# Kernel tuning notes

Hardware: AMD Instinct MI355X
Metric: run time of the kernel (lower is better)

Reference implementation:

```python
import jax, jax.numpy as jnp
import numpy as np

D_LOW = 32
LAGS = [1, 2, 4, 8]
# Upper-triangular pair indices (offset=1), matching torch.triu_indices(d_low, d_low, 1)
IDX_I, IDX_J = np.triu_indices(D_LOW, k=1)
IDX_I = jnp.asarray(IDX_I)
IDX_J = jnp.asarray(IDX_J)
EPS = 1e-6


def setup_inputs() -> dict:
    key = jax.random.key(0)
    ks = jax.random.split(key, 7)
    b, n, d_model = 4, 4096, 1024
    d_plucker = D_LOW * (D_LOW - 1) // 2  # 496
    s = lambda fan_in: 1.0 / np.sqrt(fan_in)
    return {
        "x": jax.random.normal(ks[0], (b, n, d_model), dtype=jnp.float32),
        "W_red": jax.random.normal(ks[1], (d_model, D_LOW), dtype=jnp.float32) * s(d_model),
        "b_red": jax.random.normal(ks[2], (D_LOW,), dtype=jnp.float32) * s(d_model),
        "W_exp": jax.random.normal(ks[3], (d_plucker, d_model), dtype=jnp.float32) * s(d_plucker),
        "b_exp": jax.random.normal(ks[4], (d_model,), dtype=jnp.float32) * s(d_plucker),
        "W_gate": jax.random.normal(ks[5], (2 * d_model, d_model), dtype=jnp.float32) * s(2 * d_model),
        "b_gate": jax.random.normal(ks[6], (d_model,), dtype=jnp.float32) * s(2 * d_model),
    }


def reference(x, W_red, b_red, W_exp, b_exp, W_gate, b_gate):
    b, n, _ = x.shape
    d_plucker = D_LOW * (D_LOW - 1) // 2
    z = x @ W_red + b_red  # [b, n, d_low]
    plucker_total = jnp.zeros((b, n, d_plucker), dtype=x.dtype)
    counts = jnp.zeros((b, n, 1), dtype=x.dtype)
    for lag in LAGS:
        if lag <= 0 or lag >= n:
            continue
        z_curr = z[:, lag:, :]   # [b, n-lag, d_low]
        z_past = z[:, :-lag, :]  # [b, n-lag, d_low]
        # Antisymmetric Plucker coordinates over upper-triangular index pairs
        p = (z_curr[:, :, IDX_I] * z_past[:, :, IDX_J]
             - z_curr[:, :, IDX_J] * z_past[:, :, IDX_I])  # [b, n-lag, d_plucker]
        norm = jnp.linalg.norm(p, axis=-1, keepdims=True)
        p = p / jnp.maximum(norm, EPS)
        plucker_total = plucker_total.at[:, lag:, :].add(p)
        counts = counts.at[:, lag:, :].add(1.0)
    counts = jnp.maximum(counts, 1.0)
    plucker_avg = plucker_total / counts
    g_avg = plucker_avg @ W_exp + b_exp  # [b, n, d_model]
    concat = jnp.concatenate([x, g_avg], axis=-1)  # [b, n, 2*d_model]
    gate = jax.nn.sigmoid(concat @ W_gate + b_gate)
    return gate * x + (1.0 - gate) * g_avg
```

## Files before the change

kernel.cpp:

```cpp
#include <hip/hip_runtime.h>
#include <hip/hip_bf16.h>
#include <math.h>

#define B_DIM   4
#define N_DIM   4096
#define D_MODEL 1024
#define D_LOW   32
#define NPAIR   496
#define NROWS   (B_DIM * N_DIM)
#define KPAD3   512
#define LDA2    1536

typedef __bf16 bf16;
typedef __bf16 bf16x8 __attribute__((ext_vector_type(8)));
typedef __bf16 bf16x4 __attribute__((ext_vector_type(4)));
typedef float  f32x4  __attribute__((ext_vector_type(4)));

#define GLOAD_LDS16(g, l) __builtin_amdgcn_global_load_lds( \
    (__attribute__((address_space(1))) void*)(g),           \
    (__attribute__((address_space(3))) void*)(l), 16, 0, 0)

__global__ __launch_bounds__(256) void prep_misc(const float* __restrict__ Wr,
                                                 bf16* __restrict__ WrT,
                                                 const float* __restrict__ We,
                                                 const float* __restrict__ be,
                                                 bf16* __restrict__ WeB) {
    __shared__ float tile[32][33];
    const int bx = blockIdx.x;
    const int t  = threadIdx.x;
    if (bx < 32) {
        const int kb = bx * 32;
        {
            int k = t >> 3, c4 = (t & 7) * 4;
            float4 v = *reinterpret_cast<const float4*>(&Wr[(size_t)(kb + k) * 32 + c4]);
            tile[k][c4 + 0] = v.x; tile[k][c4 + 1] = v.y;
            tile[k][c4 + 2] = v.z; tile[k][c4 + 3] = v.w;
        }
        __syncthreads();
        {
            int c = t >> 3, kq = (t & 7) * 4;
            bf16x4 o = { (bf16)tile[kq + 0][c], (bf16)tile[kq + 1][c],
                         (bf16)tile[kq + 2][c], (bf16)tile[kq + 3][c] };
            *reinterpret_cast<bf16x4*>(&WrT[(size_t)c * 1024 + kb + kq]) = o;
        }
    } else {
        size_t o = ((size_t)(bx - 32) * 256 + t) * 4;
        int row = (int)(o >> 10), col = (int)(o & 1023);
        float4 v = {0.f, 0.f, 0.f, 0.f};
        if (row < NPAIR)       v = *reinterpret_cast<const float4*>(&We[(size_t)row * 1024 + col]);
        else if (row == NPAIR) v = *reinterpret_cast<const float4*>(&be[col]);
        bf16x4 b = { (bf16)v.x, (bf16)v.y, (bf16)v.z, (bf16)v.w };
        *reinterpret_cast<bf16x4*>(&WeB[o]) = b;
    }
}

__global__ __launch_bounds__(256) void k1_mfma(const float* __restrict__ x,
                                               const bf16* __restrict__ WrT,
                                               bf16* __restrict__ a2,
                                               float* __restrict__ zpart) {
    const int t    = threadIdx.x;
    const int wv   = t >> 6, lane = t & 63;
    const int l15  = lane & 15, lhi = lane >> 4;
    const int kc   = blockIdx.x;
    const int mt   = blockIdx.y;
    const int row  = mt * 64 + wv * 16 + l15;
    const int kb   = kc * 256;

    f32x4 accz[2] = { (f32x4){0.f,0.f,0.f,0.f}, (f32x4){0.f,0.f,0.f,0.f} };

#pragma unroll
    for (int ks = 0; ks < 8; ++ks) {
        const int k0 = kb + ks * 32 + lhi * 8;
        const float4 u0 = *reinterpret_cast<const float4*>(&x[(size_t)row * 1024 + k0]);
        const float4 u1 = *reinterpret_cast<const float4*>(&x[(size_t)row * 1024 + k0 + 4]);
        bf16x8 af = { (bf16)u0.x, (bf16)u0.y, (bf16)u0.z, (bf16)u0.w,
                      (bf16)u1.x, (bf16)u1.y, (bf16)u1.z, (bf16)u1.w };
        *reinterpret_cast<bf16x8*>(&a2[(size_t)row * LDA2 + k0]) = af;
        const bf16x8 b0 = *reinterpret_cast<const bf16x8*>(
            &WrT[(size_t)l15 * 1024 + kb + ks * 32 + lhi * 8]);
        const bf16x8 b1 = *reinterpret_cast<const bf16x8*>(
            &WrT[(size_t)(16 + l15) * 1024 + kb + ks * 32 + lhi * 8]);
        accz[0] = __builtin_amdgcn_mfma_f32_16x16x32_bf16(af, b0, accz[0], 0, 0, 0);
        accz[1] = __builtin_amdgcn_mfma_f32_16x16x32_bf16(af, b1, accz[1], 0, 0, 0);
    }
#pragma unroll
    for (int cg = 0; cg < 2; ++cg)
#pragma unroll
        for (int r = 0; r < 4; ++r) {
            const int rout = mt * 64 + wv * 16 + lhi * 4 + r;
            zpart[((size_t)kc * NROWS + rout) * 32 + cg * 16 + l15] = accz[cg][r];
        }
}

__global__ __launch_bounds__(256) void k2_plucker(const float* __restrict__ zpart,
                                                  const float* __restrict__ br,
                                                  bf16* __restrict__ a2) {
    const int wv   = threadIdx.x >> 6;
    const int lane = threadIdx.x & 63;
    const int row  = blockIdx.x * 4 + wv;
    const int t    = row & (N_DIM - 1);
    const int c    = lane & 31;
    const float bias = br[c];

    float zc = bias;
#pragma unroll
    for (int p = 0; p < 4; ++p)
        zc += zpart[((size_t)p * NROWS + row) * 32 + c];

    float zp[4];
    float red[9];
    red[0] = zc * zc;
#pragma unroll
    for (int li = 0; li < 4; ++li) {
        const int lag = 1 << li;
        float v = 0.f;
        if (t >= lag) {
            v = bias;
#pragma unroll
            for (int p = 0; p < 4; ++p)
                v += zpart[((size_t)p * NROWS + (row - lag)) * 32 + c];
        }
        zp[li] = v;
        red[1 + li] = zc * zp[li];
        red[5 + li] = zp[li] * zp[li];
    }
#pragma unroll
    for (int m = 1; m < 32; m <<= 1) {
#pragma unroll
        for (int i = 0; i < 9; ++i) red[i] += __shfl_xor(red[i], m);
    }
    float cnt = 0.f;
#pragma unroll
    for (int li = 0; li < 4; ++li) cnt += (t >= (1 << li)) ? 1.f : 0.f;
    const float inv = 1.f / fmaxf(cnt, 1.f);

    float w = 0.f;
#pragma unroll
    for (int li = 0; li < 4; ++li) {
        float n2 = fmaxf(red[0] * red[5 + li] - red[1 + li] * red[1 + li], 0.f);
        float nr = sqrtf(n2);
        float s  = (t >= (1 << li)) ? inv / fmaxf(nr, 1e-6f) : 0.f;
        w += s * zp[li];
    }

#pragma unroll
    for (int u = 0; u < 8; ++u) {
        const int k = u * 64 + lane;
        float v = 0.f;
        if (k < NPAIR) {
            int kk = k, i = 0;
            while (kk >= 31 - i) { kk -= 31 - i; ++i; }
            const int j = i + 1 + kk;
            float zci = __shfl(zc, i), zcj = __shfl(zc, j);
            float wi  = __shfl(w, i),  wj  = __shfl(w, j);
            v = zci * wj - zcj * wi;
        }
        a2[(size_t)row * LDA2 + 1024 + k] = (bf16)v;
    }
}

__global__ __launch_bounds__(256) void transpose2(const float* __restrict__ Wg,
                                                  const float* __restrict__ We,
                                                  bf16* __restrict__ BcT,
                                                  bf16* __restrict__ WgbT,
                                                  bf16* __restrict__ WeT) {
    __shared__ float tile[32][36];
    const int z = blockIdx.z;
    const float* src = (z == 0) ? Wg : (z == 1) ? (Wg + (size_t)1024 * 1024) : We;
    bf16* dst  = (z == 0) ? BcT : (z == 1) ? WgbT : WeT;
    const int Kpad = (z == 0) ? 1536 : (z == 1) ? 1024 : 512;
    const int Ksrc = (z == 2) ? NPAIR : 1024;
    const int kb = blockIdx.x * 32;
    if (kb >= Kpad) return;
    const int nb = blockIdx.y * 32;
    const int t  = threadIdx.x;
    int li = t * 4;
    int kl = li >> 5, nl = li & 31;
    float4 v = {0.f, 0.f, 0.f, 0.f};
    if (kb + kl < Ksrc)
        v = *reinterpret_cast<const float4*>(&src[(size_t)(kb + kl) * 1024 + nb + nl]);
    tile[kl][nl + 0] = v.x; tile[kl][nl + 1] = v.y;
    tile[kl][nl + 2] = v.z; tile[kl][nl + 3] = v.w;
    __syncthreads();
    int nl2 = li >> 5, kl2 = li & 31;
    bf16x4 o = { (bf16)tile[kl2 + 0][nl2], (bf16)tile[kl2 + 1][nl2],
                 (bf16)tile[kl2 + 2][nl2], (bf16)tile[kl2 + 3][nl2] };
    *reinterpret_cast<bf16x4*>(&dst[(size_t)(nb + nl2) * Kpad + kb + kl2]) = o;
}

__global__ __launch_bounds__(256) void wcomb_wave(const bf16* __restrict__ WgbT,
                                                  const bf16* __restrict__ WeB,
                                                  bf16* __restrict__ BcT) {
    const int t    = threadIdx.x;
    const int wv   = t >> 6, lane = t & 63;
    const int l15  = lane & 15, lhi = lane >> 4;
    const int kk0  = blockIdx.x * 16;
    const int n0   = blockIdx.y * 64 + wv * 16;
    f32x4 acc = (f32x4){0.f, 0.f, 0.f, 0.f};
#pragma unroll 8
    for (int kb = 0; kb < 1024; kb += 32) {
        const bf16x8 af = *reinterpret_cast<const bf16x8*>(
            &WgbT[(size_t)(n0 + l15) * 1024 + kb + lhi * 8]);
        const bf16x8 bf = *reinterpret_cast<const bf16x8*>(
            &WeB[(size_t)(kk0 + l15) * 1024 + kb + lhi * 8]);
        acc = __builtin_amdgcn_mfma_f32_16x16x32_bf16(af, bf, acc, 0, 0, 0);
    }
#pragma unroll
    for (int r = 0; r < 4; ++r) {
        const int n = n0 + lhi * 4 + r;
        BcT[(size_t)n * 1536 + 1024 + kk0 + l15] = (bf16)acc[r];
    }
}

__global__ __launch_bounds__(256, 2) void gemmfu(const bf16* __restrict__ A,
                                                 const bf16* __restrict__ Bt,
                                                 const bf16* __restrict__ WeT,
                                                 const float* __restrict__ bg,
                                                 const float* __restrict__ be,
                                                 float* __restrict__ out) {
    extern __shared__ char lds[];
    const int t    = threadIdx.x;
    const int w    = t >> 6, lane = t & 63;
    const int wr   = w >> 1, wc = w & 1;
    const int l15  = lane & 15, lhi = lane >> 4;

    const int fid = blockIdx.x;
    const int xcd = fid & 7, loc = fid >> 3;
    const int mb  = (xcd * 16 + (loc >> 3)) * 128;
    const int nb  = (loc & 7) * 128;

    char* const ldsA = lds;
    char* const ldsB = lds + 32768;

    const int srow1 = t >> 3;
    const int scol1 = ((t & 7) ^ (srow1 & 7)) * 8;
    const size_t aOff1 = (size_t)(mb + srow1) * LDA2 + scol1;
    const size_t bOff1 = (size_t)(nb + srow1) * 1536 + scol1;
#define STAGE1(d, kb) do { \
    _Pragma("unroll") for (int q = 0; q < 4; ++q) \
        GLOAD_LDS16(A + aOff1 + (size_t)(q * 32) * LDA2 + (kb), \
                    ldsA + (d) * 16384 + q * 4096 + t * 16); \
    _Pragma("unroll") for (int q = 0; q < 4; ++q) \
        GLOAD_LDS16(Bt + bOff1 + (size_t)(q * 32) * 1536 + (kb), \
                    ldsB + (d) * 16384 + q * 4096 + t * 16); } while (0)

    const int srow2 = t >> 2;
    const int scol2 = ((t & 3) ^ ((srow2 >> 1) & 3)) * 8;
    const size_t aOff2 = (size_t)(mb + srow2) * LDA2 + 1024 + scol2;
    const size_t bOff2 = (size_t)(nb + srow2) * 1536 + 1024 + scol2;
    const size_t wOff2 = (size_t)(nb + srow2) * 512 + scol2;
#define STAGE2(d, kb) do { \
    GLOAD_LDS16(A + aOff2 + (kb),                        ldsA + (d) * 16384 + t * 16); \
    GLOAD_LDS16(A + aOff2 + (size_t)64 * LDA2 + (kb),    ldsA + (d) * 16384 + 4096 + t * 16); \
    GLOAD_LDS16(Bt + bOff2 + (kb),                       ldsB + (d) * 16384 + t * 16); \
    GLOAD_LDS16(Bt + bOff2 + (size_t)64 * 1536 + (kb),   ldsB + (d) * 16384 + 4096 + t * 16); \
    GLOAD_LDS16(WeT + wOff2 + (kb),                      ldsB + (d) * 16384 + 8192 + t * 16); \
    GLOAD_LDS16(WeT + wOff2 + (size_t)64 * 512 + (kb),   ldsB + (d) * 16384 + 8192 + 4096 + t * 16); } while (0)

    const int swx1 = (l15 & 7) << 4;
    const int swr2 = ((l15 >> 1) & 3) << 4;

    f32x4 acc[4][4], acc2[4][4];
#pragma unroll
    for (int i = 0; i < 4; ++i)
#pragma unroll
        for (int j = 0; j < 4; ++j) {
            acc[i][j]  = (f32x4){0.f, 0.f, 0.f, 0.f};
            acc2[i][j] = (f32x4){0.f, 0.f, 0.f, 0.f};
        }
    bf16x8 afr[4][2], bfr[4][2];

    STAGE1(0, 0);

    for (int kt = 0; kt < 16; ++kt) {
        const int d = kt & 1;
        asm volatile("s_barrier" ::: "memory");
        if (kt < 15) {
            STAGE1(d ^ 1, (kt + 1) * 64);
            asm volatile("s_waitcnt vmcnt(8)" ::: "memory");
        } else {
            STAGE2(d ^ 1, 0);
            asm volatile("s_waitcnt vmcnt(6)" ::: "memory");
        }
        asm volatile("s_barrier" ::: "memory");

        const char* Ab = ldsA + d * 16384;
        const char* Bb = ldsB + d * 16384;
#pragma unroll
        for (int mf = 0; mf < 4; ++mf)
#pragma unroll
            for (int ks = 0; ks < 2; ++ks) {
                int lin = (wr * 64 + mf * 16 + l15) * 128 + ks * 64 + lhi * 16;
                afr[mf][ks] = *reinterpret_cast<const bf16x8*>(Ab + (lin ^ swx1));
            }
#pragma unroll
        for (int nf = 0; nf < 4; ++nf)
#pragma unroll
            for (int ks = 0; ks < 2; ++ks) {
                int lin = (wc * 64 + nf * 16 + l15) * 128 + ks * 64 + lhi * 16;
                bfr[nf][ks] = *reinterpret_cast<const bf16x8*>(Bb + (lin ^ swx1));
            }
        __builtin_amdgcn_s_setprio(1);
#pragma unroll
        for (int mf = 0; mf < 4; ++mf)
#pragma unroll
            for (int nf = 0; nf < 4; ++nf)
#pragma unroll
                for (int ks = 0; ks < 2; ++ks)
                    acc[mf][nf] = __builtin_amdgcn_mfma_f32_16x16x32_bf16(
                        afr[mf][ks], bfr[nf][ks], acc[mf][nf], 0, 0, 0);
        __builtin_amdgcn_s_setprio(0);
    }

    for (int ft = 0; ft < 16; ++ft) {
        const int d = ft & 1;
        asm volatile("s_barrier" ::: "memory");
        if (ft < 15) {
            STAGE2(d ^ 1, (ft + 1) * 32);
            asm volatile("s_waitcnt vmcnt(6)" ::: "memory");
        } else {
            asm volatile("s_waitcnt vmcnt(0)" ::: "memory");
        }
        asm volatile("s_barrier" ::: "memory");

        const char* Ab = ldsA + d * 16384;
        const char* Bb = ldsB + d * 16384;
        bf16x8 a2f[4], bcf[4], wef[4];
#pragma unroll
        for (int mf = 0; mf < 4; ++mf) {
            int lin = (wr * 64 + mf * 16 + l15) * 64 + ((lhi * 16) ^ swr2);
            a2f[mf] = *reinterpret_cast<const bf16x8*>(Ab + lin);
        }
#pragma unroll
        for (int nf = 0; nf < 4; ++nf) {
            int lin = (wc * 64 + nf * 16 + l15) * 64 + ((lhi * 16) ^ swr2);
            bcf[nf] = *reinterpret_cast<const bf16x8*>(Bb + lin);
            wef[nf] = *reinterpret_cast<const bf16x8*>(Bb + 8192 + lin);
        }
        __builtin_amdgcn_s_setprio(1);
#pragma unroll
        for (int mf = 0; mf < 4; ++mf)
#pragma unroll
            for (int nf = 0; nf < 4; ++nf) {
                acc[mf][nf]  = __builtin_amdgcn_mfma_f32_16x16x32_bf16(
                    a2f[mf], bcf[nf], acc[mf][nf], 0, 0, 0);
                acc2[mf][nf] = __builtin_amdgcn_mfma_f32_16x16x32_bf16(
                    a2f[mf], wef[nf], acc2[mf][nf], 0, 0, 0);
            }
        __builtin_amdgcn_s_setprio(0);
    }

#pragma unroll
    for (int mf = 0; mf < 4; ++mf) {
#pragma unroll
        for (int nf = 0; nf < 4; ++nf) {
            const int col = nb + wc * 64 + nf * 16 + l15;
            const float bgate = bg[col] + (float)Bt[(size_t)col * 1536 + 1024 + NPAIR];
            const float bexp  = be[col];
#pragma unroll
            for (int r = 0; r < 4; ++r) {
                const int row = mb + wr * 64 + mf * 16 + lhi * 4 + r;
                const float s    = acc[mf][nf][r] + bgate;
                const float gate = 1.f / (1.f + expf(-s));
                const float g    = acc2[mf][nf][r] + bexp;
                const float xv   = (float)A[(size_t)row * LDA2 + col];
                out[(size_t)row * D_MODEL + col] = gate * xv + (1.f - gate) * g;
            }
        }
    }
}

extern "C" void kernel_launch(void* const* d_in, const int* in_sizes, int n_in,
                              void* d_out, int out_size, void* d_ws, size_t ws_size,
                              hipStream_t stream) {
    const float* x  = (const float*)d_in[0];
    const float* Wr = (const float*)d_in[1];
    const float* br = (const float*)d_in[2];
    const float* We = (const float*)d_in[3];
    const float* be = (const float*)d_in[4];
    const float* Wg = (const float*)d_in[5];
    const float* bg = (const float*)d_in[6];
    float* out = (float*)d_out;

    char* ws = (char*)d_ws;
    float* zpart = (float*)(ws);
    bf16*  A2    = (bf16*)(ws + (32u << 20));
    bf16*  WeT   = (bf16*)(ws + (80u << 20));
    bf16*  BcT   = (bf16*)(ws + (81u << 20));
    bf16*  WgbT  = (bf16*)(ws + (84u << 20));
    bf16*  WeB   = (bf16*)(ws + (86u << 20));
    bf16*  WrT   = (bf16*)(ws + (88u << 20));

    (void)hipFuncSetAttribute(reinterpret_cast<const void*>(&gemmfu),
                              hipFuncAttributeMaxDynamicSharedMemorySize, 65536);

    prep_misc<<<544, 256, 0, stream>>>(Wr, WrT, We, be, WeB);
    transpose2<<<dim3(32, 32, 3), 256, 0, stream>>>(Wg, We, BcT, WgbT, WeT);
    wcomb_wave<<<dim3(32, 16), 256, 0, stream>>>(WgbT, WeB, BcT);
    k1_mfma<<<dim3(4, 256), 256, 0, stream>>>(x, WrT, A2, zpart);
    k2_plucker<<<NROWS / 4, 256, 0, stream>>>(zpart, br, A2);

    gemmfu<<<1024, 256, 65536, stream>>>(A2, BcT, WeT, bg, be, out);
}
```

Before: 153.1 us.

## Fuse z projection and Plucker kernels via LDS and merge weight-prep launches

```diff
diff --git a/kernel.cpp b/kernel.cpp
--- a/kernel.cpp
+++ b/kernel.cpp
@@ -20,152 +20,47 @@
     (__attribute__((address_space(1))) void*)(g),           \
     (__attribute__((address_space(3))) void*)(l), 16, 0, 0)
 
-__global__ __launch_bounds__(256) void prep_misc(const float* __restrict__ Wr,
-                                                 bf16* __restrict__ WrT,
-                                                 const float* __restrict__ We,
-                                                 const float* __restrict__ be,
-                                                 bf16* __restrict__ WeB) {
-    __shared__ float tile[32][33];
-    const int bx = blockIdx.x;
-    const int t  = threadIdx.x;
-    if (bx < 32) {
-        const int kb = bx * 32;
-        {
-            int k = t >> 3, c4 = (t & 7) * 4;
-            float4 v = *reinterpret_cast<const float4*>(&Wr[(size_t)(kb + k) * 32 + c4]);
-            tile[k][c4 + 0] = v.x; tile[k][c4 + 1] = v.y;
-            tile[k][c4 + 2] = v.z; tile[k][c4 + 3] = v.w;
-        }
-        __syncthreads();
-        {
-            int c = t >> 3, kq = (t & 7) * 4;
-            bf16x4 o = { (bf16)tile[kq + 0][c], (bf16)tile[kq + 1][c],
-                         (bf16)tile[kq + 2][c], (bf16)tile[kq + 3][c] };
-            *reinterpret_cast<bf16x4*>(&WrT[(size_t)c * 1024 + kb + kq]) = o;
-        }
-    } else {
-        size_t o = ((size_t)(bx - 32) * 256 + t) * 4;
-        int row = (int)(o >> 10), col = (int)(o & 1023);
-        float4 v = {0.f, 0.f, 0.f, 0.f};
-        if (row < NPAIR)       v = *reinterpret_cast<const float4*>(&We[(size_t)row * 1024 + col]);
-        else if (row == NPAIR) v = *reinterpret_cast<const float4*>(&be[col]);
-        bf16x4 b = { (bf16)v.x, (bf16)v.y, (bf16)v.z, (bf16)v.w };
-        *reinterpret_cast<bf16x4*>(&WeB[o]) = b;
-    }
-}
-
-__global__ __launch_bounds__(256) void k1_mfma(const float* __restrict__ x,
-                                               const bf16* __restrict__ WrT,
-                                               bf16* __restrict__ a2,
-                                               float* __restrict__ zpart) {
-    const int t    = threadIdx.x;
-    const int wv   = t >> 6, lane = t & 63;
-    const int l15  = lane & 15, lhi = lane >> 4;
-    const int kc   = blockIdx.x;
-    const int mt   = blockIdx.y;
-    const int row  = mt * 64 + wv * 16 + l15;
-    const int kb   = kc * 256;
-
-    f32x4 accz[2] = { (f32x4){0.f,0.f,0.f,0.f}, (f32x4){0.f,0.f,0.f,0.f} };
-
-#pragma unroll
-    for (int ks = 0; ks < 8; ++ks) {
-        const int k0 = kb + ks * 32 + lhi * 8;
-        const float4 u0 = *reinterpret_cast<const float4*>(&x[(size_t)row * 1024 + k0]);
-        const float4 u1 = *reinterpret_cast<const float4*>(&x[(size_t)row * 1024 + k0 + 4]);
-        bf16x8 af = { (bf16)u0.x, (bf16)u0.y, (bf16)u0.z, (bf16)u0.w,
-                      (bf16)u1.x, (bf16)u1.y, (bf16)u1.z, (bf16)u1.w };
-        *reinterpret_cast<bf16x8*>(&a2[(size_t)row * LDA2 + k0]) = af;
-        const bf16x8 b0 = *reinterpret_cast<const bf16x8*>(
-            &WrT[(size_t)l15 * 1024 + kb + ks * 32 + lhi * 8]);
-        const bf16x8 b1 = *reinterpret_cast<const bf16x8*>(
-            &WrT[(size_t)(16 + l15) * 1024 + kb + ks * 32 + lhi * 8]);
-        accz[0] = __builtin_amdgcn_mfma_f32_16x16x32_bf16(af, b0, accz[0], 0, 0, 0);
-        accz[1] = __builtin_amdgcn_mfma_f32_16x16x32_bf16(af, b1, accz[1], 0, 0, 0);
-    }
-#pragma unroll
-    for (int cg = 0; cg < 2; ++cg)
-#pragma unroll
-        for (int r = 0; r < 4; ++r) {
-            const int rout = mt * 64 + wv * 16 + lhi * 4 + r;
-            zpart[((size_t)kc * NROWS + rout) * 32 + cg * 16 + l15] = accz[cg][r];
-        }
-}
-
-__global__ __launch_bounds__(256) void k2_plucker(const float* __restrict__ zpart,
-                                                  const float* __restrict__ br,
-                                                  bf16* __restrict__ a2) {
-    const int wv   = threadIdx.x >> 6;
-    const int lane = threadIdx.x & 63;
-    const int row  = blockIdx.x * 4 + wv;
-    const int t    = row & (N_DIM - 1);
-    const int c    = lane & 31;
-    const float bias = br[c];
-
-    float zc = bias;
-#pragma unroll
-    for (int p = 0; p < 4; ++p)
-        zc += zpart[((size_t)p * NROWS + row) * 32 + c];
-
-    float zp[4];
-    float red[9];
-    red[0] = zc * zc;
-#pragma unroll
-    for (int li = 0; li < 4; ++li) {
-        const int lag = 1 << li;
-        float v = 0.f;
-        if (t >= lag) {
-            v = bias;
-#pragma unroll
-            for (int p = 0; p < 4; ++p)
-                v += zpart[((size_t)p * NROWS + (row - lag)) * 32 + c];
-        }
-        zp[li] = v;
-        red[1 + li] = zc * zp[li];
-        red[5 + li] = zp[li] * zp[li];
-    }
-#pragma unroll
-    for (int m = 1; m < 32; m <<= 1) {
-#pragma unroll
-        for (int i = 0; i < 9; ++i) red[i] += __shfl_xor(red[i], m);
-    }
-    float cnt = 0.f;
-#pragma unroll
-    for (int li = 0; li < 4; ++li) cnt += (t >= (1 << li)) ? 1.f : 0.f;
-    const float inv = 1.f / fmaxf(cnt, 1.f);
-
-    float w = 0.f;
-#pragma unroll
-    for (int li = 0; li < 4; ++li) {
-        float n2 = fmaxf(red[0] * red[5 + li] - red[1 + li] * red[1 + li], 0.f);
-        float nr = sqrtf(n2);
-        float s  = (t >= (1 << li)) ? inv / fmaxf(nr, 1e-6f) : 0.f;
-        w += s * zp[li];
-    }
-
-#pragma unroll
-    for (int u = 0; u < 8; ++u) {
-        const int k = u * 64 + lane;
-        float v = 0.f;
-        if (k < NPAIR) {
-            int kk = k, i = 0;
-            while (kk >= 31 - i) { kk -= 31 - i; ++i; }
-            const int j = i + 1 + kk;
-            float zci = __shfl(zc, i), zcj = __shfl(zc, j);
-            float wi  = __shfl(w, i),  wj  = __shfl(w, j);
-            v = zci * wj - zcj * wi;
-        }
-        a2[(size_t)row * LDA2 + 1024 + k] = (bf16)v;
-    }
-}
-
-__global__ __launch_bounds__(256) void transpose2(const float* __restrict__ Wg,
+__global__ __launch_bounds__(256) void transpose3(const float* __restrict__ Wg,
                                                   const float* __restrict__ We,
+                                                  const float* __restrict__ Wr,
+                                                  const float* __restrict__ be,
                                                   bf16* __restrict__ BcT,
                                                   bf16* __restrict__ WgbT,
-                                                  bf16* __restrict__ WeT) {
+                                                  bf16* __restrict__ WeT,
+                                                  bf16* __restrict__ WrT,
+                                                  bf16* __restrict__ WeB) {
     __shared__ float tile[32][36];
     const int z = blockIdx.z;
+    const int t = threadIdx.x;
+    if (z == 3) {
+        const int flat = blockIdx.y * 32 + blockIdx.x;
+        if (flat >= 544) return;
+        if (flat < 32) {
+            const int kb = flat * 32;
+            {
+                int k = t >> 3, c4 = (t & 7) * 4;
+                float4 v = *reinterpret_cast<const float4*>(&Wr[(size_t)(kb + k) * 32 + c4]);
+                tile[k][c4 + 0] = v.x; tile[k][c4 + 1] = v.y;
+                tile[k][c4 + 2] = v.z; tile[k][c4 + 3] = v.w;
+            }
+            __syncthreads();
+            {
+                int c = t >> 3, kq = (t & 7) * 4;
+                bf16x4 o = { (bf16)tile[kq + 0][c], (bf16)tile[kq + 1][c],
+                             (bf16)tile[kq + 2][c], (bf16)tile[kq + 3][c] };
+                *reinterpret_cast<bf16x4*>(&WrT[(size_t)c * 1024 + kb + kq]) = o;
+            }
+        } else {
+            size_t o = ((size_t)(flat - 32) * 256 + t) * 4;
+            int row = (int)(o >> 10), col = (int)(o & 1023);
+            float4 v = {0.f, 0.f, 0.f, 0.f};
+            if (row < NPAIR)       v = *reinterpret_cast<const float4*>(&We[(size_t)row * 1024 + col]);
+            else if (row == NPAIR) v = *reinterpret_cast<const float4*>(&be[col]);
+            bf16x4 b = { (bf16)v.x, (bf16)v.y, (bf16)v.z, (bf16)v.w };
+            *reinterpret_cast<bf16x4*>(&WeB[o]) = b;
+        }
+        return;
+    }
     const float* src = (z == 0) ? Wg : (z == 1) ? (Wg + (size_t)1024 * 1024) : We;
     bf16* dst  = (z == 0) ? BcT : (z == 1) ? WgbT : WeT;
     const int Kpad = (z == 0) ? 1536 : (z == 1) ? 1024 : 512;
@@ -173,7 +68,6 @@
     const int kb = blockIdx.x * 32;
     if (kb >= Kpad) return;
     const int nb = blockIdx.y * 32;
-    const int t  = threadIdx.x;
     int li = t * 4;
     int kl = li >> 5, nl = li & 31;
     float4 v = {0.f, 0.f, 0.f, 0.f};
@@ -212,6 +106,102 @@
     }
 }
 
+__global__ __launch_bounds__(256) void k12(const float* __restrict__ x,
+                                           const bf16* __restrict__ WrT,
+                                           const float* __restrict__ br,
+                                           bf16* __restrict__ a2) {
+    __shared__ float z_lds[80][32];
+    const int t    = threadIdx.x;
+    const int wv   = t >> 6, lane = t & 63;
+    const int l15  = lane & 15, lhi = lane >> 4;
+    const int mt   = blockIdx.x;
+    const int base = mt * 64;
+
+    for (int tile = wv; tile < 5; tile += 4) {
+        if (tile == 0 && (mt & 63) == 0) continue;
+        const bool ghost = (tile == 0);
+        const int row = base - 16 + tile * 16 + l15;
+        f32x4 accz[2] = { (f32x4){0.f,0.f,0.f,0.f}, (f32x4){0.f,0.f,0.f,0.f} };
+#pragma unroll 4
+        for (int ks = 0; ks < 32; ++ks) {
+            const int k0 = ks * 32 + lhi * 8;
+            const float4 u0 = *reinterpret_cast<const float4*>(&x[(size_t)row * 1024 + k0]);
+            const float4 u1 = *reinterpret_cast<const float4*>(&x[(size_t)row * 1024 + k0 + 4]);
+            bf16x8 af = { (bf16)u0.x, (bf16)u0.y, (bf16)u0.z, (bf16)u0.w,
+                          (bf16)u1.x, (bf16)u1.y, (bf16)u1.z, (bf16)u1.w };
+            if (!ghost)
+                *reinterpret_cast<bf16x8*>(&a2[(size_t)row * LDA2 + k0]) = af;
+            const bf16x8 b0 = *reinterpret_cast<const bf16x8*>(
+                &WrT[(size_t)l15 * 1024 + k0]);
+            const bf16x8 b1 = *reinterpret_cast<const bf16x8*>(
+                &WrT[(size_t)(16 + l15) * 1024 + k0]);
+            accz[0] = __builtin_amdgcn_mfma_f32_16x16x32_bf16(af, b0, accz[0], 0, 0, 0);
+            accz[1] = __builtin_amdgcn_mfma_f32_16x16x32_bf16(af, b1, accz[1], 0, 0, 0);
+        }
+#pragma unroll
+        for (int cg = 0; cg < 2; ++cg)
+#pragma unroll
+            for (int r = 0; r < 4; ++r)
+                z_lds[tile * 16 + lhi * 4 + r][cg * 16 + l15] = accz[cg][r];
+    }
+    __syncthreads();
+
+    const int c = lane & 31;
+    const float bias = br[c];
+    for (int i = 0; i < 16; ++i) {
+        const int r_loc = wv * 16 + i;
+        const int row   = base + r_loc;
+        const int tpos  = row & (N_DIM - 1);
+
+        float zc = z_lds[16 + r_loc][c] + bias;
+        float zp[4];
+        float red[9];
+        red[0] = zc * zc;
+#pragma unroll
+        for (int li = 0; li < 4; ++li) {
+            const int lag = 1 << li;
+            float v = 0.f;
+            if (tpos >= lag) v = z_lds[16 + r_loc - lag][c] + bias;
+            zp[li] = v;
+            red[1 + li] = zc * zp[li];
+            red[5 + li] = zp[li] * zp[li];
+        }
+#pragma unroll
+        for (int m = 1; m < 32; m <<= 1) {
+#pragma unroll
+            for (int q = 0; q < 9; ++q) red[q] += __shfl_xor(red[q], m);
+        }
+        float cnt = 0.f;
+#pragma unroll
+        for (int li = 0; li < 4; ++li) cnt += (tpos >= (1 << li)) ? 1.f : 0.f;
+        const float inv = 1.f / fmaxf(cnt, 1.f);
+
+        float w = 0.f;
+#pragma unroll
+        for (int li = 0; li < 4; ++li) {
+            float n2 = fmaxf(red[0] * red[5 + li] - red[1 + li] * red[1 + li], 0.f);
+            float nr = sqrtf(n2);
+            float s  = (tpos >= (1 << li)) ? inv / fmaxf(nr, 1e-6f) : 0.f;
+            w += s * zp[li];
+        }
+
+#pragma unroll
+        for (int u = 0; u < 8; ++u) {
+            const int k = u * 64 + lane;
+            float v = 0.f;
+            if (k < NPAIR) {
+                int kk = k, ii = 0;
+                while (kk >= 31 - ii) { kk -= 31 - ii; ++ii; }
+                const int j = ii + 1 + kk;
+                float zci = __shfl(zc, ii), zcj = __shfl(zc, j);
+                float wi  = __shfl(w, ii),  wj  = __shfl(w, j);
+                v = zci * wj - zcj * wi;
+            }
+            a2[(size_t)row * LDA2 + 1024 + k] = (bf16)v;
+        }
+    }
+}
+
 __global__ __launch_bounds__(256, 2) void gemmfu(const bf16* __restrict__ A,
                                                  const bf16* __restrict__ Bt,
                                                  const bf16* __restrict__ WeT,
@@ -383,7 +373,6 @@
     float* out = (float*)d_out;
 
     char* ws = (char*)d_ws;
-    float* zpart = (float*)(ws);
     bf16*  A2    = (bf16*)(ws + (32u << 20));
     bf16*  WeT   = (bf16*)(ws + (80u << 20));
     bf16*  BcT   = (bf16*)(ws + (81u << 20));
@@ -394,11 +383,9 @@
     (void)hipFuncSetAttribute(reinterpret_cast<const void*>(&gemmfu),
                               hipFuncAttributeMaxDynamicSharedMemorySize, 65536);
 
-    prep_misc<<<544, 256, 0, stream>>>(Wr, WrT, We, be, WeB);
-    transpose2<<<dim3(32, 32, 3), 256, 0, stream>>>(Wg, We, BcT, WgbT, WeT);
+    transpose3<<<dim3(32, 32, 4), 256, 0, stream>>>(Wg, We, Wr, be,
+                                                    BcT, WgbT, WeT, WrT, WeB);
     wcomb_wave<<<dim3(32, 16), 256, 0, stream>>>(WgbT, WeB, BcT);
-    k1_mfma<<<dim3(4, 256), 256, 0, stream>>>(x, WrT, A2, zpart);
-    k2_plucker<<<NROWS / 4, 256, 0, stream>>>(zpart, br, A2);
-
+    k12<<<256, 256, 0, stream>>>(x, WrT, br, A2);
     gemmfu<<<1024, 256, 65536, stream>>>(A2, BcT, WeT, bg, be, out);
 }
```

New measurement: 219.2 us. 43.2% more time.
